# Optimization experiments

Hardware: AMD Instinct MI355X
Metric: run time of the kernel (lower is better)

Reference implementation:

```python
import jax, jax.numpy as jnp
import numpy as np

TAU = 0.5

def setup_inputs() -> dict:
    key = jax.random.key(0)
    kx, ky = jax.random.split(key)
    B, H = 8192, 256
    x = jax.random.normal(kx, (B, H), dtype=jnp.float32)
    y = jax.random.normal(ky, (B, H), dtype=jnp.float32)
    return {"x": x, "y": y}

def reference(x, y):
    # L2-normalize rows
    x_norm = x / jnp.linalg.norm(x, axis=1, keepdims=True)
    y_norm = y / jnp.linalg.norm(y, axis=1, keepdims=True)
    xy_norm = jnp.concatenate([x_norm, y_norm], axis=0)  # [2N, H]
    yx_norm = jnp.concatenate([y_norm, x_norm], axis=0)  # [2N, H]
    # [2N, 2N] cosine-similarity matrix (dominant memory traffic)
    sim_mat_1 = xy_norm @ xy_norm.T
    exp_mat = jnp.exp(sim_mat_1 / TAU)
    exp_row_sum = jnp.sum(exp_mat, axis=1)
    exp_diag = jnp.diagonal(exp_mat)
    denominator = exp_row_sum - exp_diag
    # diag(xy_norm @ yx_norm.T) is the row-wise dot product (avoids redundant NxN matmul)
    pos_sim = jnp.sum(xy_norm * yx_norm, axis=1)
    numerator = jnp.exp(pos_sim / TAU)
    nt_xent = -jnp.log(numerator / denominator)
    return jnp.mean(nt_xent)
```

## Files before the change

kernel.cpp:

```cpp
#include <hip/hip_runtime.h>
#include <hip/hip_bf16.h>
#include <math.h>

constexpr int NROWS = 8192;
constexpr int HDIM  = 256;
constexpr int N2    = 16384;
constexpr int TM    = 256;
constexpr int BK    = 32;
constexpr int NCHUNK = HDIM / BK;
constexpr int NTILE = N2 / TM;
constexpr int NBLK  = NTILE * (NTILE + 1) / 2;

constexpr float PRESCALE = 1.69864357f;

typedef __attribute__((ext_vector_type(4))) float floatx4;
typedef __attribute__((ext_vector_type(8))) short shortx8;

__device__ __forceinline__ void async_copy16(const void* gptr, void* lptr) {
    __builtin_amdgcn_global_load_lds(
        (const __attribute__((address_space(1))) unsigned int*)gptr,
        (__attribute__((address_space(3))) unsigned int*)lptr, 16, 0, 0);
}

#define WAIT_VM4()   __builtin_amdgcn_s_waitcnt(0x0F74)
#define WAIT_VM0()   __builtin_amdgcn_s_waitcnt(0x0F70)
#define MEMFENCE()   __asm__ __volatile__("" ::: "memory")
#define RAW_BARRIER() do { MEMFENCE(); __builtin_amdgcn_s_barrier(); MEMFENCE(); } while (0)

#define DPP_ROW_SHL_ADD(v, CTRL) do {                                        \
    union { float f; int i; } _u, _r; _u.f = (v);                            \
    _r.i = __builtin_amdgcn_update_dpp(0, _u.i, (CTRL), 0xF, 0xF, true);     \
    (v) += _r.f; } while (0)

__global__ __launch_bounds__(256) void normalize_kernel(
    const float* __restrict__ x, const float* __restrict__ y,
    __hip_bfloat16* __restrict__ Z, float* __restrict__ pos,
    float* __restrict__ rowsum, float* __restrict__ out)
{
    const int wave = threadIdx.x >> 6, lane = threadIdx.x & 63;
    const int row  = blockIdx.x * 4 + wave;

    const float4 xv = ((const float4*)x)[row * 64 + lane];
    const float4 yv = ((const float4*)y)[row * 64 + lane];

    float sx  = xv.x*xv.x + xv.y*xv.y + xv.z*xv.z + xv.w*xv.w;
    float sy  = yv.x*yv.x + yv.y*yv.y + yv.z*yv.z + yv.w*yv.w;
    float sxy = xv.x*yv.x + xv.y*yv.y + xv.z*yv.z + xv.w*yv.w;
    #pragma unroll
    for (int m = 1; m < 64; m <<= 1) {
        sx  += __shfl_xor(sx,  m);
        sy  += __shfl_xor(sy,  m);
        sxy += __shfl_xor(sxy, m);
    }
    const float rxn = rsqrtf(sx), ryn = rsqrtf(sy);
    const float rx = rxn * PRESCALE, ry = ryn * PRESCALE;

    union { ushort4 u; __hip_bfloat16 h[4]; } zx, zy;
    zx.h[0] = __float2bfloat16(xv.x * rx); zx.h[1] = __float2bfloat16(xv.y * rx);
    zx.h[2] = __float2bfloat16(xv.z * rx); zx.h[3] = __float2bfloat16(xv.w * rx);
    zy.h[0] = __float2bfloat16(yv.x * ry); zy.h[1] = __float2bfloat16(yv.y * ry);
    zy.h[2] = __float2bfloat16(yv.z * ry); zy.h[3] = __float2bfloat16(yv.w * ry);
    ((ushort4*)Z)[row * 64 + lane]             = zx.u;
    ((ushort4*)Z)[(row + NROWS) * 64 + lane]   = zy.u;

    if (lane == 0) {
        const float p = sxy * rxn * ryn;
        pos[row]         = p;
        pos[row + NROWS] = p;
    }
    const int gt = blockIdx.x * 256 + threadIdx.x;
    if (gt < N2) rowsum[gt] = 0.f;
    if (gt == 0) out[0] = 0.f;
}

__global__ __launch_bounds__(512, 2) void simgemm_kernel(
    const __hip_bfloat16* __restrict__ Z, float* __restrict__ rowsum)
{
    const int b = blockIdx.x;
    const int k = b & 7;
    const int m = b >> 3;
    int bi, bj;
    if (m < 36) {
        int ti = (int)((17.0f - sqrtf(289.0f - 8.0f * (float)m)) * 0.5f);
        if (m < ti * (17 - ti) / 2) ti--;
        else if (m >= (ti + 1) * (16 - ti) / 2) ti++;
        const int tj = ti + (m - ti * (17 - ti) / 2);
        bi = k * 8 + ti;
        bj = k * 8 + tj;
    } else {
        const int m2 = m - 36;
        const int hh = m2 >> 5;
        const int r  = m2 & 31;
        const int h  = hh * 8 + k;
        const int q  = h >> 1;
        const int sub = h & 1;
        int gi = 0;
        #pragma unroll
        for (int t = 6; t > 0; --t)
            if (q >= t * (15 - t) / 2) { gi = t; break; }
        const int gj = gi + 1 + (q - gi * (15 - gi) / 2);
        bi = gi * 8 + sub * 4 + (r >> 3);
        bj = gj * 8 + (r & 7);
    }
    const bool diag = (bi == bj);

    __shared__ alignas(16) __hip_bfloat16 tiles[6 * TM * BK];
    __shared__ float rs[TM];
    __shared__ float cs[TM];
    __hip_bfloat16* tA = tiles;
    __hip_bfloat16* tB = tiles + TM * BK;

    const int tid  = threadIdx.x;
    const int wave = tid >> 6;
    const int lane = tid & 63;
    const int wm   = wave & 1;
    const int wn   = wave >> 1;
    const int g    = lane >> 4;
    const int m15  = lane & 15;

    if (tid < TM) { rs[tid] = 0.f; cs[tid] = 0.f; }

    const int st_r0  = wave * 32 + (lane >> 2);
    const int st_c   = (lane & 3) ^ ((lane >> 3) & 3);
    const __hip_bfloat16* gA0 = Z + (size_t)(bi * TM + st_r0) * HDIM + st_c * 8;
    const __hip_bfloat16* gA1 = gA0 + 16 * HDIM;
    const __hip_bfloat16* gB0 = Z + (size_t)(bj * TM + st_r0) * HDIM + st_c * 8;
    const __hip_bfloat16* gB1 = gB0 + 16 * HDIM;
    __hip_bfloat16* lA0 = tA + (wave * 32) * BK;
    __hip_bfloat16* lA1 = tA + (wave * 32 + 16) * BK;
    __hip_bfloat16* lB0 = tB + (wave * 32) * BK;
    __hip_bfloat16* lB1 = tB + (wave * 32 + 16) * BK;

    const int sw = g ^ ((m15 >> 1) & 3);
    const __hip_bfloat16* rA = tA + (wm * 128 + m15) * BK + sw * 8;
    const __hip_bfloat16* rB = tB + (wn * 64  + m15) * BK + sw * 8;

    floatx4 acc[8][4] = {};

    #define STAGE(ck)  do {                                                  \
        const int _o = ((ck) % 3) * 2 * TM * BK;                             \
        async_copy16(gA0 + (ck) * BK, lA0 + _o);                             \
        async_copy16(gA1 + (ck) * BK, lA1 + _o);                             \
        async_copy16(gB0 + (ck) * BK, lB0 + _o);                             \
        async_copy16(gB1 + (ck) * BK, lB1 + _o);                             \
    } while (0)

    STAGE(0);

    #pragma unroll
    for (int s = 0; s < NCHUNK; ++s) {
        if (s + 1 < NCHUNK) { STAGE(s + 1); WAIT_VM4(); }
        else                { WAIT_VM0(); }
        RAW_BARRIER();

        const int bo = (s % 3) * 2 * TM * BK;
        shortx8 af[8], bfr[4];
        #pragma unroll
        for (int f = 0; f < 8; ++f)
            af[f]  = *(const shortx8*)(rA + bo + f * 16 * BK);
        #pragma unroll
        for (int f = 0; f < 4; ++f)
            bfr[f] = *(const shortx8*)(rB + bo + f * 16 * BK);

        __builtin_amdgcn_s_setprio(1);
        #pragma unroll
        for (int fm = 0; fm < 8; ++fm)
            #pragma unroll
            for (int fn = 0; fn < 4; ++fn)
                acc[fm][fn] = __builtin_amdgcn_mfma_f32_16x16x32_bf16(
                    af[fm], bfr[fn], acc[fm][fn], 0, 0, 0);
        __builtin_amdgcn_s_setprio(0);
    }
    #undef STAGE

    float rp[8][4] = {{0.f}};
    float cp[4]    = {0.f};

    if (!diag) {
        #pragma unroll
        for (int fm = 0; fm < 8; ++fm)
            #pragma unroll
            for (int fn = 0; fn < 4; ++fn) {
                const floatx4 a = acc[fm][fn];
                #pragma unroll
                for (int q = 0; q < 4; ++q) {
                    const float e = __builtin_amdgcn_exp2f(a[q]);
                    rp[fm][q] += e;
                    cp[fn]    += e;
                }
            }
    } else {
        #pragma unroll
        for (int fm = 0; fm < 8; ++fm)
            #pragma unroll
            for (int fn = 0; fn < 4; ++fn) {
                const floatx4 a = acc[fm][fn];
                const int cl = wn * 64 + fn * 16 + m15;
                #pragma unroll
                for (int q = 0; q < 4; ++q) {
                    const int rl = wm * 128 + fm * 16 + g * 4 + q;
                    float e = __builtin_amdgcn_exp2f(a[q]);
                    if (cl <= rl) e = 0.f;
                    rp[fm][q] += e;
                    cp[fn]    += e;
                }
            }
    }

    #pragma unroll
    for (int fm = 0; fm < 8; ++fm)
        #pragma unroll
        for (int q = 0; q < 4; ++q) {
            float v = rp[fm][q];
            DPP_ROW_SHL_ADD(v, 0x101);
            DPP_ROW_SHL_ADD(v, 0x102);
            DPP_ROW_SHL_ADD(v, 0x104);
            DPP_ROW_SHL_ADD(v, 0x108);
            rp[fm][q] = v;
        }
    if (m15 == 0) {
        #pragma unroll
        for (int fm = 0; fm < 8; ++fm)
            #pragma unroll
            for (int q = 0; q < 4; ++q)
                atomicAdd(&rs[wm * 128 + fm * 16 + g * 4 + q], rp[fm][q]);
    }

    #pragma unroll
    for (int mask = 16; mask < 64; mask <<= 1)
        #pragma unroll
        for (int fn = 0; fn < 4; ++fn)
            cp[fn] += __shfl_xor(cp[fn], mask);
    if (g == 0) {
        #pragma unroll
        for (int fn = 0; fn < 4; ++fn)
            atomicAdd(&cs[wn * 64 + fn * 16 + m15], cp[fn]);
    }

    __syncthreads();
    if (tid < TM) {
        atomicAdd(&rowsum[(size_t)bi * TM + tid], rs[tid]);
        atomicAdd(&rowsum[(size_t)bj * TM + tid], cs[tid]);
    }
}

__global__ __launch_bounds__(1024) void finalize_kernel(
    const float* __restrict__ rowsum, const float* __restrict__ pos,
    float* __restrict__ out)
{
    const int i = threadIdx.x + blockIdx.x * 1024;
    float s = logf(rowsum[i]) - 2.0f * pos[i];
    #pragma unroll
    for (int off = 32; off; off >>= 1) s += __shfl_down(s, off);
    __shared__ float sh[16];
    const int lt = threadIdx.x;
    if ((lt & 63) == 0) sh[lt >> 6] = s;
    __syncthreads();
    if (lt == 0) {
        float tot = 0.f;
        #pragma unroll
        for (int w = 0; w < 16; ++w) tot += sh[w];
        atomicAdd(out, tot / (float)N2);
    }
}

extern "C" void kernel_launch(void* const* d_in, const int* in_sizes, int n_in,
                              void* d_out, int out_size, void* d_ws, size_t ws_size,
                              hipStream_t stream)
{
    const float* x = (const float*)d_in[0];
    const float* y = (const float*)d_in[1];

    __hip_bfloat16* Z = (__hip_bfloat16*)d_ws;
    float* rowsum = (float*)((char*)d_ws + (size_t)N2 * HDIM * sizeof(__hip_bfloat16));
    float* pos    = rowsum + N2;

    normalize_kernel<<<NROWS / 4, 256, 0, stream>>>(x, y, Z, pos, rowsum, (float*)d_out);
    simgemm_kernel<<<NBLK, 512, 0, stream>>>(Z, rowsum);
    finalize_kernel<<<N2 / 1024, 1024, 0, stream>>>(rowsum, pos, (float*)d_out);
}
```

Baseline: 155.6 us.

## Restructure GEMM main loop into fine-grained half-tile phases with deeper async prefetch

Replaces the 3-slot, one-chunk-ahead K loop with an explicitly unrolled 16-phase schedule over 8 LDS pieces. Each K sub-chunk is split into two halves of the M fragments, and each phase issues one async global-to-LDS piece load. Waitcnt gates are placed so several pieces stay in flight while MFMAs run. The aim is to hide global load latency better and to interleave LDS reads, copies and MFMAs. In exchange it uses more LDS and two barriers per phase, which may add synchronisation overhead and reduce occupancy.

After: 165.9 us. 6.6% more time.

```diff
diff --git a/kernel.cpp b/kernel.cpp
--- a/kernel.cpp
+++ b/kernel.cpp
@@ -6,8 +6,8 @@
 constexpr int HDIM  = 256;
 constexpr int N2    = 16384;
 constexpr int TM    = 256;
-constexpr int BK    = 32;
-constexpr int NCHUNK = HDIM / BK;
+constexpr int KSUB  = 32;
+constexpr int PIECE = TM * KSUB;
 constexpr int NTILE = N2 / TM;
 constexpr int NBLK  = NTILE * (NTILE + 1) / 2;
 
@@ -22,8 +22,9 @@
         (__attribute__((address_space(3))) unsigned int*)lptr, 16, 0, 0);
 }
 
-#define WAIT_VM4()   __builtin_amdgcn_s_waitcnt(0x0F74)
-#define WAIT_VM0()   __builtin_amdgcn_s_waitcnt(0x0F70)
+#define GATE(IMM)    __builtin_amdgcn_s_waitcnt(IMM)
+#define NOGATE       ((void)0)
+#define NOSTAGE      ((void)0)
 #define MEMFENCE()   __asm__ __volatile__("" ::: "memory")
 #define RAW_BARRIER() do { MEMFENCE(); __builtin_amdgcn_s_barrier(); MEMFENCE(); } while (0)
 
@@ -104,11 +105,9 @@
     }
     const bool diag = (bi == bj);
 
-    __shared__ alignas(16) __hip_bfloat16 tiles[6 * TM * BK];
+    __shared__ alignas(16) __hip_bfloat16 tiles[8 * PIECE];
     __shared__ float rs[TM];
     __shared__ float cs[TM];
-    __hip_bfloat16* tA = tiles;
-    __hip_bfloat16* tB = tiles + TM * BK;
 
     const int tid  = threadIdx.x;
     const int wave = tid >> 6;
@@ -120,58 +119,81 @@
 
     if (tid < TM) { rs[tid] = 0.f; cs[tid] = 0.f; }
 
-    const int st_r0  = wave * 32 + (lane >> 2);
-    const int st_c   = (lane & 3) ^ ((lane >> 3) & 3);
-    const __hip_bfloat16* gA0 = Z + (size_t)(bi * TM + st_r0) * HDIM + st_c * 8;
-    const __hip_bfloat16* gA1 = gA0 + 16 * HDIM;
-    const __hip_bfloat16* gB0 = Z + (size_t)(bj * TM + st_r0) * HDIM + st_c * 8;
-    const __hip_bfloat16* gB1 = gB0 + 16 * HDIM;
-    __hip_bfloat16* lA0 = tA + (wave * 32) * BK;
-    __hip_bfloat16* lA1 = tA + (wave * 32 + 16) * BK;
-    __hip_bfloat16* lB0 = tB + (wave * 32) * BK;
-    __hip_bfloat16* lB1 = tB + (wave * 32 + 16) * BK;
+    const int st_r0 = wave * 32 + (lane >> 2);
+    const int st_c  = (lane & 3) ^ ((lane >> 3) & 3);
+    const __hip_bfloat16* gA = Z + (size_t)(bi * TM + st_r0) * HDIM + st_c * 8;
+    const __hip_bfloat16* gB = Z + (size_t)(bj * TM + st_r0) * HDIM + st_c * 8;
+
+    #define STAGE_P(SLOT, GSRC, KK) do {                                      \
+        __hip_bfloat16* _lp = tiles + (SLOT) * PIECE + (wave * 32) * KSUB;    \
+        async_copy16((GSRC) + (KK), _lp);                                     \
+        async_copy16((GSRC) + (KK) + 16 * HDIM, _lp + 16 * KSUB);             \
+    } while (0)
 
     const int sw = g ^ ((m15 >> 1) & 3);
-    const __hip_bfloat16* rA = tA + (wm * 128 + m15) * BK + sw * 8;
-    const __hip_bfloat16* rB = tB + (wn * 64  + m15) * BK + sw * 8;
+    const int raOff = (wm * 128 + m15) * KSUB + sw * 8;
+    const int rbOff = (wn * 64  + m15) * KSUB + sw * 8;
 
     floatx4 acc[8][4] = {};
-
-    #define STAGE(ck)  do {                                                  \
-        const int _o = ((ck) % 3) * 2 * TM * BK;                             \
-        async_copy16(gA0 + (ck) * BK, lA0 + _o);                             \
-        async_copy16(gA1 + (ck) * BK, lA1 + _o);                             \
-        async_copy16(gB0 + (ck) * BK, lB0 + _o);                             \
-        async_copy16(gB1 + (ck) * BK, lB1 + _o);                             \
+    shortx8 bfr[4];
+
+    #define PHASE(BUF, KS, FMH, STAGES, GATES) do {                           \
+        const __hip_bfloat16* _ra = tiles + ((BUF)*4 + (KS)) * PIECE + raOff; \
+        shortx8 _af[4];                                                       \
+        _Pragma("unroll")                                                     \
+        for (int _f = 0; _f < 4; ++_f)                                        \
+            _af[_f] = *(const shortx8*)(_ra + ((FMH)*4 + _f) * 16 * KSUB);    \
+        if ((FMH) == 0) {                                                     \
+            const __hip_bfloat16* _rb =                                       \
+                tiles + ((BUF)*4 + 2 + (KS)) * PIECE + rbOff;                 \
+            _Pragma("unroll")                                                 \
+            for (int _f = 0; _f < 4; ++_f)                                    \
+                bfr[_f] = *(const shortx8*)(_rb + _f * 16 * KSUB);            \
+        }                                                                     \
+        STAGES;                                                               \
+        GATES;                                                                \
+        RAW_BARRIER();                                           \
+        __builtin_amdgcn_s_setprio(1);                                        \
+        _Pragma("unroll")                                                     \
+        for (int _i = 0; _i < 4; ++_i)                                        \
+            _Pragma("unroll")                                                 \
+            for (int _j = 0; _j < 4; ++_j)                                    \
+                acc[(FMH)*4 + _i][_j] = __builtin_amdgcn_mfma_f32_16x16x32_bf16( \
+                    _af[_i], bfr[_j], acc[(FMH)*4 + _i][_j], 0, 0, 0);        \
+        __builtin_amdgcn_s_setprio(0);                                        \
+        __builtin_amdgcn_sched_barrier(0);                                    \
+        RAW_BARRIER();                                          \
     } while (0)
 
-    STAGE(0);
-
-    #pragma unroll
-    for (int s = 0; s < NCHUNK; ++s) {
-        if (s + 1 < NCHUNK) { STAGE(s + 1); WAIT_VM4(); }
-        else                { WAIT_VM0(); }
-        RAW_BARRIER();
-
-        const int bo = (s % 3) * 2 * TM * BK;
-        shortx8 af[8], bfr[4];
-        #pragma unroll
-        for (int f = 0; f < 8; ++f)
-            af[f]  = *(const shortx8*)(rA + bo + f * 16 * BK);
-        #pragma unroll
-        for (int f = 0; f < 4; ++f)
-            bfr[f] = *(const shortx8*)(rB + bo + f * 16 * BK);
-
-        __builtin_amdgcn_s_setprio(1);
-        #pragma unroll
-        for (int fm = 0; fm < 8; ++fm)
-            #pragma unroll
-            for (int fn = 0; fn < 4; ++fn)
-                acc[fm][fn] = __builtin_amdgcn_mfma_f32_16x16x32_bf16(
-                    af[fm], bfr[fn], acc[fm][fn], 0, 0, 0);
-        __builtin_amdgcn_s_setprio(0);
-    }
-    #undef STAGE
+    STAGE_P(2, gB, 0);
+    STAGE_P(0, gA, 0);
+    STAGE_P(3, gB, 32);
+    STAGE_P(1, gA, 32);
+    STAGE_P(6, gB, 64);
+    STAGE_P(4, gA, 64);
+    STAGE_P(7, gB, 96);
+    GATE(0x0F7A);
+    RAW_BARRIER();
+
+    PHASE(0,0,0, STAGE_P(5, gA,  96), NOGATE);
+    PHASE(0,0,1, STAGE_P(2, gB, 128), GATE(0x0F7A));
+    PHASE(0,1,0, STAGE_P(0, gA, 128), NOGATE);
+    PHASE(0,1,1, STAGE_P(3, gB, 160), GATE(0x0F7A));
+    PHASE(1,0,0, STAGE_P(1, gA, 160), NOGATE);
+    PHASE(1,0,1, STAGE_P(6, gB, 192), GATE(0x0F7A));
+    PHASE(1,1,0, STAGE_P(4, gA, 192), NOGATE);
+    PHASE(1,1,1, STAGE_P(7, gB, 224), GATE(0x0F7A));
+    PHASE(0,0,0, STAGE_P(5, gA, 224), NOGATE);
+    PHASE(0,0,1, NOSTAGE,             GATE(0x0F78));
+    PHASE(0,1,0, NOSTAGE,             NOGATE);
+    PHASE(0,1,1, NOSTAGE,             GATE(0x0F74));
+    PHASE(1,0,0, NOSTAGE,             NOGATE);
+    PHASE(1,0,1, NOSTAGE,             GATE(0x0F70));
+    PHASE(1,1,0, NOSTAGE,             NOGATE);
+    PHASE(1,1,1, NOSTAGE,             NOGATE);
+
+    #undef PHASE
+    #undef STAGE_P
 
     float rp[8][4] = {{0.f}};
     float cp[4]    = {0.f};
```
